# Kernel tuning notes

Measured on AMD Instinct MI355X. Metric: run time of the kernel, lower is better.

Reference implementation:

```python
import jax, jax.numpy as jnp
import numpy as np

B, N, FEAT, HID, K, GH, GW = 4, 4096, 64, 128, 16, 256, 256


def setup_inputs() -> dict:
    key = jax.random.key(0)
    ks = jax.random.split(key, 16)
    # N distinct grid cells per batch -> unique sparse coordinates (scn active sites)
    cells = jax.vmap(lambda k: jax.random.permutation(k, GH * GW)[:N])(jax.random.split(ks[0], B))
    cy = (cells // GW).astype(jnp.float32)
    cx = (cells % GW).astype(jnp.float32)
    x = cx / GW  # round(x*GW) == cx exactly
    y = cy / GH
    z = jnp.zeros((B, N), jnp.float32)
    p = jax.random.uniform(ks[1], (B, N), jnp.float32)
    xyzp = jnp.stack([x, y, z, p], axis=-1).astype(jnp.float32)
    features = jax.random.normal(ks[2], (B, N, FEAT), jnp.float32)

    def w(k, shape, s=0.05):
        return (jax.random.normal(k, shape) * s).astype(jnp.float32)

    return {
        "xyzp": xyzp, "features": features,
        "ln_g": jnp.ones((FEAT + 2,), jnp.float32), "ln_b": jnp.zeros((FEAT + 2,), jnp.float32),
        "W1": w(ks[3], (9, FEAT + 2, HID)), "b1": jnp.zeros((HID,), jnp.float32),
        "W2": w(ks[4], (9, HID, 3 * HID)),
        "pe_w1": w(ks[5], (3, HID)), "pe_b1": jnp.zeros((HID,), jnp.float32),
        "pe_w2": w(ks[6], (HID, HID)), "pe_b2": jnp.zeros((HID,), jnp.float32),
        "at_w1": w(ks[7], (HID, HID)), "at_b1": jnp.zeros((HID,), jnp.float32),
        "at_w2": w(ks[8], (HID, HID)), "at_b2": jnp.zeros((HID,), jnp.float32),
        "ag_w": w(ks[9], (HID, FEAT)), "ag_b": jnp.zeros((FEAT,), jnp.float32),
        "mlp_w1": w(ks[10], (FEAT, HID)), "mlp_b1": jnp.zeros((HID,), jnp.float32),
        "mlp_w2": w(ks[11], (HID, FEAT)), "mlp_b2": jnp.zeros((FEAT,), jnp.float32),
    }


def _knn_gather(xf, idx):
    # xf: [B,N,C], idx: [B,N,K] -> [B,N,K,C]
    return xf[jnp.arange(xf.shape[0])[:, None, None], idx]


def _forward(xyzp, features, ln_g, ln_b, W1, b1, W2, pe_w1, pe_b1, pe_w2, pe_b2,
             at_w1, at_b1, at_w2, at_b2, ag_w, ag_b, mlp_w1, mlp_b1, mlp_w2, mlp_b2):
    # knn in (x,y,0) space -> 2D squared distances, K nearest (self included, sorted)
    xy = xyzp[..., :2]
    s = jnp.sum(xy * xy, axis=-1)
    d2 = s[:, :, None] + s[:, None, :] - 2.0 * jnp.einsum('bnd,bmd->bnm', xy, xy)
    idx = jax.lax.top_k(-d2, K)[1]  # [B,N,K]

    # positional encoding of (x,y,p) relative offsets
    xyp = jnp.stack([xyzp[..., 0], xyzp[..., 1], xyzp[..., 3]], axis=-1)  # [B,N,3]
    rel = xyp[:, :, None, :] - _knn_gather(xyp, idx)  # [B,N,K,3]
    pe = jax.nn.relu(rel @ pe_w1 + pe_b1) @ pe_w2 + pe_b2  # [B,N,K,HID]

    # polarity split + LayerNorm
    p = (xyzp[..., 3:4] - 0.5) / 0.5
    sp = jnp.concatenate([jnp.clip(p, 0.0, 1.0), -jnp.clip(p, -1.0, 0.0), features], axis=-1)
    mu = jnp.mean(sp, axis=-1, keepdims=True)
    var = jnp.var(sp, axis=-1, keepdims=True)
    sp = (sp - mu) / jnp.sqrt(var + 1e-5) * ln_g + ln_b  # [B,N,FEAT+2]

    # submanifold 3x3 conv x2 via dense index grid (active sites only)
    cy = jnp.round(xyzp[..., 1] * GH).astype(jnp.int32)
    cx = jnp.round(xyzp[..., 0] * GW).astype(jnp.int32)
    bb = jnp.broadcast_to(jnp.arange(B)[:, None], (B, N))
    grid = jnp.full((B, GH + 2, GW + 2), -1, jnp.int32)
    grid = grid.at[bb, cy + 1, cx + 1].set(jnp.broadcast_to(jnp.arange(N, dtype=jnp.int32)[None], (B, N)))
    off = jnp.arange(-1, 2)
    dy = jnp.repeat(off, 3)  # [9]
    dx = jnp.tile(off, 3)    # [9]
    bi = jnp.arange(B)[:, None, None]
    nbr = grid[bi, cy[:, :, None] + 1 + dy, cx[:, :, None] + 1 + dx]  # [B,N,9]
    mask = nbr >= 0
    safe = jnp.where(mask, nbr, 0)
    m = mask[..., None].astype(sp.dtype)

    g1 = sp[bi, safe] * m                                   # [B,N,9,FEAT+2]
    h1 = jnp.einsum('bnkc,kcd->bnd', g1, W1) + b1           # [B,N,HID]
    g2 = h1[bi, safe] * m                                   # [B,N,9,HID]
    h2 = jnp.einsum('bnkc,kcd->bnd', g2, W2)                # [B,N,3*HID]

    qkv = h2.reshape(B, N, HID, 3)  # matches torch reshape([B,N,-1,3])
    q = qkv[..., 0]
    kk = _knn_gather(qkv[..., 1], idx)
    v = _knn_gather(qkv[..., 2], idx)

    # subtraction-based vector attention scored by MLP, softmax over neighbors
    a = q[:, :, None] - kk + pe
    a = jax.nn.relu(a @ at_w1 + at_b1) @ at_w2 + at_b2
    a = jax.nn.softmax(a / jnp.sqrt(jnp.float32(HID)), axis=-2)

    res = jnp.einsum('bmnf,bmnf->bmf', a, v + pe)
    res = res @ ag_w + ag_b + features
    res = jax.nn.gelu(res @ mlp_w1 + mlp_b1, approximate=False) @ mlp_w2 + mlp_b2 + features
    return res


def reference(xyzp, features, ln_g, ln_b, W1, b1, W2, pe_w1, pe_b1, pe_w2, pe_b2,
              at_w1, at_b1, at_w2, at_b2, ag_w, ag_b, mlp_w1, mlp_b1, mlp_w2, mlp_b2):
    return _forward(xyzp, features, ln_g, ln_b, W1, b1, W2, pe_w1, pe_b1, pe_w2, pe_b2,
                    at_w1, at_b1, at_w2, at_b2, ag_w, ag_b, mlp_w1, mlp_b1, mlp_w2, mlp_b2)
```

## Files before the change

kernel.cpp:

```cpp
#include <hip/hip_runtime.h>
#include <math.h>

#define BB 4
#define NN 4096
#define FEAT 64
#define HID 128
#define KNN 16
#define GS 258
#define CIN 66

typedef __attribute__((ext_vector_type(8))) short bf16x8;
typedef __attribute__((ext_vector_type(4))) float f32x4;
#define MFMA_B16(a, b, c) __builtin_amdgcn_mfma_f32_16x16x32_bf16(a, b, c, 0, 0, 0)

__device__ __forceinline__ short f2b(float f) {
    unsigned u = __builtin_bit_cast(unsigned, f);
    u = (u + 0x7FFFu + ((u >> 16) & 1u)) >> 16;
    return (short)u;
}
__device__ __forceinline__ float b2f(short s) {
    return __builtin_bit_cast(float, ((unsigned)(unsigned short)s) << 16);
}
__device__ __forceinline__ void gload_lds16(const void* g, void* lds) {
    __builtin_amdgcn_global_load_lds((const __attribute__((address_space(1))) unsigned int*)g,
                                     (__attribute__((address_space(3))) unsigned int*)lds, 16, 0, 0);
}

__global__ void k_scatter(const float* __restrict__ xyzp, int* __restrict__ grid, int* __restrict__ cxy) {
    int i = blockIdx.x * 256 + threadIdx.x;
    if (i >= BB * NN) return;
    int b = i / NN;
    float x = xyzp[(size_t)i * 4 + 0], y = xyzp[(size_t)i * 4 + 1];
    int cx = __float2int_rn(x * 256.0f);
    int cy = __float2int_rn(y * 256.0f);
    cxy[i] = cx | (cy << 8);
    grid[b * GS * GS + (cy + 1) * GS + (cx + 1)] = i % NN;
}

__device__ __forceinline__ void ins16(unsigned* a, unsigned key) {
    if (key < a[15]) {
#pragma unroll
        for (int j = 15; j >= 1; --j) {
            unsigned prev = a[j - 1];
            a[j] = (prev > key) ? prev : ((a[j] > key) ? key : a[j]);
        }
        a[0] = a[0] < key ? a[0] : key;
    }
}

__device__ __forceinline__ void cmpex(unsigned& x, unsigned& y) {
    unsigned lo = x < y ? x : y;
    unsigned hi = x < y ? y : x;
    x = lo; y = hi;
}

__device__ __forceinline__ void merge16(const unsigned* L, unsigned* c) {
#pragma unroll
    for (int i = 0; i < 16; ++i) c[i] = L[i];
#pragma unroll
    for (int s = 0; s < 4; ++s) {
        int m = 1 << s;
        unsigned bv[16];
#pragma unroll
        for (int i = 0; i < 16; ++i) bv[i] = __shfl_xor(c[15 - i], m);
#pragma unroll
        for (int i = 0; i < 16; ++i) c[i] = c[i] < bv[i] ? c[i] : bv[i];
#pragma unroll
        for (int d = 8; d >= 1; d >>= 1)
#pragma unroll
            for (int i = 0; i < 16; ++i)
                if (!(i & d)) cmpex(c[i], c[i | d]);
    }
}

__global__ __launch_bounds__(256) void k_knn(const int* __restrict__ grid, const int* __restrict__ cxy,
                                             const float* __restrict__ xyzp, float4* __restrict__ relg) {
    int tid = threadIdx.x;
    int t = tid & 15;
    int q = blockIdx.x * 16 + (tid >> 4);
    int b = q >> 12;
    int me = cxy[q];
    int mx = me & 255, my = (me >> 8) & 255;
    const int* gb = grid + b * GS * GS;
    unsigned L[16];
#pragma unroll
    for (int j = 0; j < 16; j++) L[j] = 0xFFFFFFFFu;
    for (int i = t; i < 441; i += 16) {
        int dy = i / 21 - 10, dx = i % 21 - 10;
        int Y = my + dy, X = mx + dx;
        if ((unsigned)Y >= 256u || (unsigned)X >= 256u) continue;
        int j = gb[(Y + 1) * GS + X + 1];
        if (j >= 0) ins16(L, ((unsigned)(dx * dx + dy * dy) << 12) | (unsigned)j);
    }
    unsigned c[16];
    merge16(L, c);
    for (int r = 11; r <= 256; ++r) {
        bool need = (c[15] >> 12) >= (unsigned)(r * r);
        if (!__any(need)) break;
        if (need) {
            int rr = r * r;
            for (int dx = -r + t; dx <= r; dx += 16) {
                int X = mx + dx;
                if ((unsigned)X >= 256u) continue;
                int d2t = dx * dx + rr;
                int Y0 = my - r, Y1 = my + r;
                if ((unsigned)Y0 < 256u) {
                    int j = gb[(Y0 + 1) * GS + X + 1];
                    if (j >= 0) ins16(L, ((unsigned)d2t << 12) | (unsigned)j);
                }
                if ((unsigned)Y1 < 256u) {
                    int j = gb[(Y1 + 1) * GS + X + 1];
                    if (j >= 0) ins16(L, ((unsigned)d2t << 12) | (unsigned)j);
                }
            }
            for (int dy = -r + 1 + t; dy <= r - 1; dy += 16) {
                int Y = my + dy;
                if ((unsigned)Y >= 256u) continue;
                int rowoff = (Y + 1) * GS;
                int d2s = rr + dy * dy;
                int X0 = mx - r, X1 = mx + r;
                if ((unsigned)X0 < 256u) {
                    int j = gb[rowoff + X0 + 1];
                    if (j >= 0) ins16(L, ((unsigned)d2s << 12) | (unsigned)j);
                }
                if ((unsigned)X1 < 256u) {
                    int j = gb[rowoff + X1 + 1];
                    if (j >= 0) ins16(L, ((unsigned)d2s << 12) | (unsigned)j);
                }
            }
            merge16(L, c);
        }
    }
    unsigned mine = 0;
#pragma unroll
    for (int j = 0; j < 16; ++j)
        if (t == j) mine = c[j];
    int g = (b << 12) | (int)(mine & 4095u);
    float4 mef = *(const float4*)(xyzp + (size_t)q * 4);
    float4 tt = *(const float4*)(xyzp + (size_t)g * 4);
    float4 o;
    o.x = mef.x - tt.x; o.y = mef.y - tt.y; o.z = mef.w - tt.w;
    o.w = __int_as_float(g);
    relg[(size_t)q * 16 + t] = o;
}

#define PK128_SZ (4 * 8 * 512)
#define PKW1_SZ (9 * 3 * 8 * 512)
#define PKW2_SZ (9 * 4 * 24 * 512)

__global__ __launch_bounds__(256) void k_pack(const float* __restrict__ pe_w2, const float* __restrict__ at_w1,
                                              const float* __restrict__ at_w2, const float* __restrict__ W1,
                                              const float* __restrict__ W2,
                                              short* __restrict__ pk_pe2, short* __restrict__ pk_a1,
                                              short* __restrict__ pk_a2, short* __restrict__ pk_w1,
                                              short* __restrict__ pk_w2) {
    int i = blockIdx.x * 256 + threadIdx.x;
    if (i < 3 * PK128_SZ) {
        int seg = i / PK128_SZ, r = i % PK128_SZ;
        int f = r / 512, q = r % 512;
        int lane = q / 8, j = q % 8;
        int kt = f / 8, nt = f % 8;
        int k = kt * 32 + (lane >> 4) * 8 + j, n = nt * 16 + (lane & 15);
        const float* W = (seg == 0) ? pe_w2 : (seg == 1) ? at_w1 : at_w2;
        short* dst = (seg == 0) ? pk_pe2 : (seg == 1) ? pk_a1 : pk_a2;
        dst[r] = f2b(W[k * 128 + n]);
        return;
    }
    i -= 3 * PK128_SZ;
    if (i < PKW1_SZ) {
        int f = i / 512, q = i % 512;
        int lane = q / 8, j = q % 8;
        int tap = f / 24, rem = f % 24;
        int kt = rem / 8, nt = rem % 8;
        int k = kt * 32 + (lane >> 4) * 8 + j, n = nt * 16 + (lane & 15);
        pk_w1[i] = (k < CIN) ? f2b(W1[(tap * CIN + k) * 128 + n]) : (short)0;
        return;
    }
    i -= PKW1_SZ;
    if (i < PKW2_SZ) {
        int f = i / 512, q = i % 512;
        int lane = q / 8, j = q % 8;
        int tap = f / 96, rem = f % 96;
        int kt = rem / 24, nt = rem % 24;
        int k = kt * 32 + (lane >> 4) * 8 + j, n = nt * 16 + (lane & 15);
        pk_w2[i] = f2b(W2[((size_t)(tap * 128 + k)) * 384 + n]);
    }
}

__global__ __launch_bounds__(256) void k_fold(const float* __restrict__ pe_w2, const float* __restrict__ at_w1,
                                              const float* __restrict__ pe_b2, const float* __restrict__ at_b1,
                                              short* __restrict__ pk_wf, float* __restrict__ cf) {
    int bid = blockIdx.x;
    if (bid == 64) {
        int j = threadIdx.x;
        if (j < 128) {
            float acc = at_b1[j];
            for (int m = 0; m < 128; ++m) acc += pe_b2[m] * at_w1[m * 128 + j];
            cf[j] = acc;
        }
        return;
    }
    int idx = bid * 256 + threadIdx.x;
    int i = idx >> 7, j = idx & 127;
    float acc = 0.f;
    for (int m = 0; m < 128; ++m) acc += pe_w2[i * 128 + m] * at_w1[m * 128 + j];
    int lane = (((i >> 3) & 3) << 4) | (j & 15);
    int dst = ((i >> 5) * 8 + (j >> 4)) * 512 + lane * 8 + (i & 7);
    pk_wf[dst] = f2b(acc);
}

__global__ __launch_bounds__(256) void k_sp(const float* __restrict__ xyzp, const float* __restrict__ feat,
                                            const float* __restrict__ ln_g, const float* __restrict__ ln_b,
                                            short* __restrict__ sp_bf) {
    int i = blockIdx.x * 256 + threadIdx.x;
    if (i >= BB * NN) return;
    float v[CIN];
    float p = xyzp[(size_t)i * 4 + 3];
    float pn = (p - 0.5f) * 2.0f;
    v[0] = fminf(fmaxf(pn, 0.0f), 1.0f);
    v[1] = -fminf(fmaxf(pn, -1.0f), 0.0f);
    const float4* f4 = (const float4*)(feat + (size_t)i * FEAT);
#pragma unroll
    for (int j = 0; j < FEAT / 4; j++) {
        float4 t = f4[j];
        v[2 + 4 * j] = t.x; v[3 + 4 * j] = t.y; v[4 + 4 * j] = t.z; v[5 + 4 * j] = t.w;
    }
    float s = 0.0f;
#pragma unroll
    for (int j = 0; j < CIN; j++) s += v[j];
    float mu = s / (float)CIN;
    float vs = 0.0f;
#pragma unroll
    for (int j = 0; j < CIN; j++) { float d = v[j] - mu; vs += d * d; }
    float inv = 1.0f / sqrtf(vs / (float)CIN + 1e-5f);
    unsigned o2[64];
#pragma unroll
    for (int j = 0; j < 33; j++) {
        float a = (v[2 * j] - mu) * inv * ln_g[2 * j] + ln_b[2 * j];
        float bqq = (2 * j + 1 < CIN) ? ((v[2 * j + 1] - mu) * inv * ln_g[2 * j + 1] + ln_b[2 * j + 1]) : 0.f;
        o2[j] = (unsigned)(unsigned short)f2b(a) | (((unsigned)(unsigned short)f2b(bqq)) << 16);
    }
#pragma unroll
    for (int j = 33; j < 64; j++) o2[j] = 0;
    int4* o = (int4*)(sp_bf + (size_t)i * 128);
#pragma unroll
    for (int t = 0; t < 16; t++) o[t] = make_int4(o2[4 * t], o2[4 * t + 1], o2[4 * t + 2], o2[4 * t + 3]);
}

__global__ __launch_bounds__(256) void k_conv1(const int* __restrict__ grid, const int* __restrict__ cxy,
                                               const short* __restrict__ sp_bf, const float* __restrict__ b1,
                                               const short* __restrict__ pk_w1, const short* __restrict__ zero256,
                                               short* __restrict__ h1_bf) {
    __shared__ int sj[9][64];
    __shared__ __align__(16) char sb[2][64 * 256];
    int row0 = blockIdx.x * 64;
    int b = row0 / NN;
    int tid = threadIdx.x;
    int w = tid >> 6, l = tid & 63, cl = l & 15;
    for (int e = tid; e < 9 * 64; e += 256) {
        int k = e / 64, p = e % 64;
        int me = cxy[row0 + p];
        sj[k][p] = grid[b * GS * GS + (((me >> 8) & 255) + k / 3) * GS + ((me & 255) + k % 3)];
    }
    __syncthreads();
    f32x4 acc[4][2];
#pragma unroll
    for (int m = 0; m < 4; m++)
#pragma unroll
        for (int nt = 0; nt < 2; nt++) acc[m][nt] = (f32x4){0.f, 0.f, 0.f, 0.f};

#define STAGE1(bufp, tap)                                                                      \
    {                                                                                          \
        _Pragma("unroll") for (int i = 0; i < 4; ++i) {                                        \
            int row = w * 16 + i * 4 + (l >> 4);                                               \
            int j = sj[tap][row];                                                              \
            int srcch = cl ^ (row & 7);                                                        \
            const short* src = (j >= 0) ? (sp_bf + ((size_t)(b * NN + j) * 128 + srcch * 8))   \
                                        : (zero256 + srcch * 8);                               \
            gload_lds16(src, (bufp) + (w * 16 + i * 4) * 256);                                 \
        }                                                                                      \
    }
    STAGE1(&sb[0][0], 0);
    asm volatile("s_waitcnt vmcnt(0)" ::: "memory");
    __syncthreads();
    int cur = 0;
    for (int tap = 0; tap < 9; ++tap) {
        if (tap < 8) STAGE1(&sb[cur ^ 1][0], tap + 1);
        const char* base = &sb[cur][0];
#pragma unroll
        for (int kt = 0; kt < 3; ++kt) {
            bf16x8 a[4];
#pragma unroll
            for (int m = 0; m < 4; ++m) {
                int row = m * 16 + (l & 15);
                a[m] = *(const bf16x8*)&base[row * 256 + ((kt * 64 + (l >> 4) * 16) ^ ((row & 7) << 4))];
            }
#pragma unroll
            for (int nt = 0; nt < 2; ++nt) {
                bf16x8 bv = *(const bf16x8*)(pk_w1 + (size_t)(((tap * 3 + kt) * 8 + w * 2 + nt) * 64 + l) * 8);
#pragma unroll
                for (int m = 0; m < 4; ++m) acc[m][nt] = MFMA_B16(a[m], bv, acc[m][nt]);
            }
        }
        asm volatile("s_waitcnt vmcnt(0)" ::: "memory");
        __syncthreads();
        cur ^= 1;
    }
#pragma unroll
    for (int nt = 0; nt < 2; ++nt) {
        int col = (w * 2 + nt) * 16 + cl;
        float bb = b1[col];
#pragma unroll
        for (int m = 0; m < 4; ++m)
#pragma unroll
            for (int j = 0; j < 4; ++j) {
                int row = row0 + m * 16 + (l >> 4) * 4 + j;
                h1_bf[(size_t)row * 128 + col] = f2b(acc[m][nt][j] + bb);
            }
    }
}

__global__ __launch_bounds__(256) void k_conv2(const int* __restrict__ grid, const int* __restrict__ cxy,
                                               const short* __restrict__ h1_bf, const short* __restrict__ pk_w2,
                                               const short* __restrict__ zero256,
                                               short* __restrict__ qg, short* __restrict__ kg, short* __restrict__ vg) {
    __shared__ int sj[9][64];
    __shared__ __align__(16) char sb[2][64 * 256];
    int bid = blockIdx.x;
    int nb = bid % 3, mb = bid / 3;
    int row0 = mb * 64;
    int b = row0 / NN;
    int tid = threadIdx.x;
    int w = tid >> 6, l = tid & 63, cl = l & 15;
    for (int e = tid; e < 9 * 64; e += 256) {
        int k = e / 64, p = e % 64;
        int me = cxy[row0 + p];
        sj[k][p] = grid[b * GS * GS + (((me >> 8) & 255) + k / 3) * GS + ((me & 255) + k % 3)];
    }
    __syncthreads();
    f32x4 acc[4][2];
#pragma unroll
    for (int m = 0; m < 4; m++)
#pragma unroll
        for (int nt = 0; nt < 2; nt++) acc[m][nt] = (f32x4){0.f, 0.f, 0.f, 0.f};

#define STAGE2(bufp, tap)                                                                      \
    {                                                                                          \
        _Pragma("unroll") for (int i = 0; i < 4; ++i) {                                        \
            int row = w * 16 + i * 4 + (l >> 4);                                               \
            int j = sj[tap][row];                                                              \
            int srcch = cl ^ (row & 7);                                                        \
            const short* src = (j >= 0) ? (h1_bf + ((size_t)(b * NN + j) * 128 + srcch * 8))   \
                                        : (zero256 + srcch * 8);                               \
            gload_lds16(src, (bufp) + (w * 16 + i * 4) * 256);                                 \
        }                                                                                      \
    }
    STAGE2(&sb[0][0], 0);
    asm volatile("s_waitcnt vmcnt(0)" ::: "memory");
    __syncthreads();
    int cur = 0;
    for (int tap = 0; tap < 9; ++tap) {
        if (tap < 8) STAGE2(&sb[cur ^ 1][0], tap + 1);
        const char* base = &sb[cur][0];
#pragma unroll
        for (int kt = 0; kt < 4; ++kt) {
            bf16x8 a[4];
#pragma unroll
            for (int m = 0; m < 4; ++m) {
                int row = m * 16 + (l & 15);
                a[m] = *(const bf16x8*)&base[row * 256 + ((kt * 64 + (l >> 4) * 16) ^ ((row & 7) << 4))];
            }
#pragma unroll
            for (int nt = 0; nt < 2; ++nt) {
                bf16x8 bv = *(const bf16x8*)(pk_w2 + (size_t)(((tap * 4 + kt) * 24 + nb * 8 + w * 2 + nt) * 64 + l) * 8);
#pragma unroll
                for (int m = 0; m < 4; ++m) acc[m][nt] = MFMA_B16(a[m], bv, acc[m][nt]);
            }
        }
        asm volatile("s_waitcnt vmcnt(0)" ::: "memory");
        __syncthreads();
        cur ^= 1;
    }
#pragma unroll
    for (int nt = 0; nt < 2; ++nt) {
        int col = nb * 128 + (w * 2 + nt) * 16 + cl;
        int s = col % 3, dd = col / 3;
#pragma unroll
        for (int m = 0; m < 4; ++m)
#pragma unroll
            for (int j = 0; j < 4; ++j) {
                int row = row0 + m * 16 + (l >> 4) * 4 + j;
                if (s == 0) qg[(size_t)row * 128 + dd] = f2b(acc[m][nt][j]);
                else if (s == 1) kg[(size_t)row * 128 + dd] = f2b(acc[m][nt][j]);
                else vg[(size_t)row * 128 + (dd & 15) * 8 + (dd >> 4)] = f2b(acc[m][nt][j]);
            }
    }
}

__global__ __launch_bounds__(256) void k_qk1(const short* __restrict__ qg, const short* __restrict__ kg,
                                             const short* __restrict__ pk_a1, const float* __restrict__ cf,
                                             short* __restrict__ q1, short* __restrict__ k1) {
    __shared__ __align__(16) char sb[64 * 256];
    int bid = blockIdx.x;
    int qmode = (bid < 256);
    int row0 = (bid & 255) * 64;
    const short* S = qmode ? qg : kg;
    short* O = qmode ? q1 : k1;
    int tid = threadIdx.x;
    int w = tid >> 6, l = tid & 63, cl = l & 15;
    for (int e = tid; e < 1024; e += 256) {
        int row = e >> 4, sl = e & 15;
        gload_lds16(S + ((size_t)(row0 + row) * 128 + (sl ^ (row & 7)) * 8), &sb[e * 16]);
    }
    asm volatile("s_waitcnt vmcnt(0)" ::: "memory");
    __syncthreads();
    f32x4 acc[4][2];
#pragma unroll
    for (int m = 0; m < 4; m++)
#pragma unroll
        for (int nt = 0; nt < 2; nt++) acc[m][nt] = (f32x4){0.f, 0.f, 0.f, 0.f};
#pragma unroll
    for (int kt = 0; kt < 4; ++kt) {
        bf16x8 a[4];
#pragma unroll
        for (int m = 0; m < 4; ++m) {
            int row = m * 16 + (l & 15);
            a[m] = *(const bf16x8*)&sb[row * 256 + ((kt * 64 + (l >> 4) * 16) ^ ((row & 7) << 4))];
        }
#pragma unroll
        for (int nt = 0; nt < 2; ++nt) {
            bf16x8 bv = *(const bf16x8*)(pk_a1 + (size_t)((kt * 8 + w * 2 + nt) * 64 + l) * 8);
#pragma unroll
            for (int m = 0; m < 4; ++m) acc[m][nt] = MFMA_B16(a[m], bv, acc[m][nt]);
        }
    }
#pragma unroll
    for (int nt = 0; nt < 2; ++nt) {
        int a = w * 2 + nt;
        int col = a * 16 + cl;
        float cv = qmode ? cf[col] : 0.f;
#pragma unroll
        for (int m = 0; m < 4; ++m)
#pragma unroll
            for (int j = 0; j < 4; ++j) {
                int row = row0 + m * 16 + (l >> 4) * 4 + j;
                O[(size_t)row * 128 + cl * 8 + a] = f2b(acc[m][nt][j] + cv);
            }
    }
}

__global__ __launch_bounds__(256, 3) void k_attn(const float4* __restrict__ relg,
                                                 const short* __restrict__ q1g, const short* __restrict__ k1g,
                                                 const short* __restrict__ vg,
                                                 const float* __restrict__ pe_w1, const float* __restrict__ pe_b1,
                                                 const float* __restrict__ pe_b2, const float* __restrict__ at_b2,
                                                 const short* __restrict__ pk_pe2, const short* __restrict__ pk_wf,
                                                 const short* __restrict__ pk_a2, float* __restrict__ res1) {
    __shared__ __align__(16) char s_work[4 * 4096];
    __shared__ float4 s_rel[64];
    int tid = threadIdx.x;
    int w = tid >> 6, l = tid & 63, cl = l & 15;
    int P = blockIdx.x * 4 + w;
    char* WK = s_work + w * 4096;

    int g_reg = 0;
    if (l < 16) {
        float4 f4 = relg[(size_t)P * 16 + l];
        s_rel[w * 16 + l] = f4;
        g_reg = __float_as_int(f4.w);
    }
    bf16x8 k1f[4], vf[4];
#pragma unroll
    for (int j = 0; j < 4; ++j) {
        int g = __shfl(g_reg, (l >> 4) * 4 + j);
        k1f[j] = *(const bf16x8*)(k1g + (size_t)g * 128 + cl * 8);
        vf[j] = *(const bf16x8*)(vg + (size_t)g * 128 + cl * 8);
    }
    bf16x8 q1f = *(const bf16x8*)(q1g + (size_t)P * 128 + cl * 8);
    {
        int c0 = 2 * l;
        float wa0 = pe_w1[c0], wa1 = pe_w1[c0 + 1];
        float wb0 = pe_w1[128 + c0], wb1 = pe_w1[129 + c0];
        float wc0 = pe_w1[256 + c0], wc1 = pe_w1[257 + c0];
        float ba0 = pe_b1[c0], ba1 = pe_b1[c0 + 1];
#pragma unroll
        for (int lr = 0; lr < 16; ++lr) {
            float4 rel = s_rel[w * 16 + lr];
            float h0 = fmaxf(rel.x * wa0 + rel.y * wb0 + rel.z * wc0 + ba0, 0.f);
            float h1v = fmaxf(rel.x * wa1 + rel.y * wb1 + rel.z * wc1 + ba1, 0.f);
            unsigned pk = (unsigned)(unsigned short)f2b(h0) | (((unsigned)(unsigned short)f2b(h1v)) << 16);
            *(unsigned*)&WK[lr * 256 + ((4 * l) ^ ((lr & 7) << 4))] = pk;
        }
    }
    int ra = l & 15;
    unsigned pe_pk[8][2];
    {
        f32x4 pacc[8];
#pragma unroll
        for (int nt = 0; nt < 8; nt++) pacc[nt] = (f32x4){0.f, 0.f, 0.f, 0.f};
#pragma unroll
        for (int kt = 0; kt < 4; ++kt) {
            int off = kt * 64 + (l >> 4) * 16;
            bf16x8 a0 = *(const bf16x8*)&WK[ra * 256 + (off ^ ((ra & 7) << 4))];
#pragma unroll
            for (int nt = 0; nt < 8; ++nt) {
                bf16x8 bv = *(const bf16x8*)(pk_pe2 + (size_t)((kt * 8 + nt) * 64 + l) * 8);
                pacc[nt] = MFMA_B16(a0, bv, pacc[nt]);
            }
        }
#pragma unroll
        for (int nt = 0; nt < 8; ++nt) {
            float b2v = pe_b2[nt * 16 + cl];
            float p0v = pacc[nt][0] + b2v, p1v = pacc[nt][1] + b2v;
            float p2v = pacc[nt][2] + b2v, p3v = pacc[nt][3] + b2v;
            pe_pk[nt][0] = (unsigned)(unsigned short)f2b(p0v) | (((unsigned)(unsigned short)f2b(p1v)) << 16);
            pe_pk[nt][1] = (unsigned)(unsigned short)f2b(p2v) | (((unsigned)(unsigned short)f2b(p3v)) << 16);
        }
    }
    f32x4 facc[8];
#pragma unroll
    for (int nt = 0; nt < 8; nt++) facc[nt] = (f32x4){0.f, 0.f, 0.f, 0.f};
#pragma unroll
    for (int kt = 0; kt < 4; ++kt) {
        int off = kt * 64 + (l >> 4) * 16;
        bf16x8 a0 = *(const bf16x8*)&WK[ra * 256 + (off ^ ((ra & 7) << 4))];
#pragma unroll
        for (int nt = 0; nt < 8; ++nt) {
            bf16x8 bv = *(const bf16x8*)(pk_wf + (size_t)((kt * 8 + nt) * 64 + l) * 8);
            facc[nt] = MFMA_B16(a0, bv, facc[nt]);
        }
    }
#pragma unroll
    for (int nt = 0; nt < 8; ++nt) {
        int col = nt * 16 + cl;
        float qv = b2f(q1f[nt]);
#pragma unroll
        for (int j = 0; j < 4; ++j) {
            int lr = (l >> 4) * 4 + j;
            float x = facc[nt][j] + qv - b2f(k1f[j][nt]);
            *(short*)&WK[lr * 256 + ((col * 2) ^ ((lr & 7) << 4))] = f2b(fmaxf(x, 0.f));
        }
    }
#pragma unroll
    for (int nt = 0; nt < 8; nt++) facc[nt] = (f32x4){0.f, 0.f, 0.f, 0.f};
#pragma unroll
    for (int kt = 0; kt < 4; ++kt) {
        int off = kt * 64 + (l >> 4) * 16;
        bf16x8 a0 = *(const bf16x8*)&WK[ra * 256 + (off ^ ((ra & 7) << 4))];
#pragma unroll
        for (int nt = 0; nt < 8; ++nt) {
            bf16x8 bv = *(const bf16x8*)(pk_a2 + (size_t)((kt * 8 + nt) * 64 + l) * 8);
            facc[nt] = MFMA_B16(a0, bv, facc[nt]);
        }
    }
    const float scale = 0.08838834764831845f;
#pragma unroll
    for (int nt = 0; nt < 8; ++nt) {
        int col = nt * 16 + cl;
        float bv = at_b2[col];
        float vv[4];
#pragma unroll
        for (int j = 0; j < 4; ++j) vv[j] = (facc[nt][j] + bv) * scale;
        float m = fmaxf(fmaxf(vv[0], vv[1]), fmaxf(vv[2], vv[3]));
        m = fmaxf(m, __shfl_xor(m, 16));
        m = fmaxf(m, __shfl_xor(m, 32));
        float ee[4], es = 0.f;
#pragma unroll
        for (int j = 0; j < 4; ++j) { ee[j] = __expf(vv[j] - m); es += ee[j]; }
        es += __shfl_xor(es, 16);
        es += __shfl_xor(es, 32);
        float pev[4];
        pev[0] = b2f((short)(pe_pk[nt][0] & 0xffff));
        pev[1] = b2f((short)(pe_pk[nt][0] >> 16));
        pev[2] = b2f((short)(pe_pk[nt][1] & 0xffff));
        pev[3] = b2f((short)(pe_pk[nt][1] >> 16));
        float o = 0.f;
#pragma unroll
        for (int j = 0; j < 4; ++j) o += ee[j] * (b2f(vf[j][nt]) + pev[j]);
        o += __shfl_xor(o, 16);
        o += __shfl_xor(o, 32);
        if (l < 16) res1[(size_t)P * 128 + col] = o / es;
    }
}

__global__ __launch_bounds__(256) void k_head(const float* __restrict__ res1, const float* __restrict__ feat,
                                              const float* __restrict__ ag_w, const float* __restrict__ ag_b,
                                              const float* __restrict__ mlp_w1, const float* __restrict__ mlp_b1,
                                              const float* __restrict__ mlp_w2, const float* __restrict__ mlp_b2,
                                              float* __restrict__ out) {
    __shared__ __align__(16) float rs[64][128];
    __shared__ __align__(16) float r1s[64][64];
    int tid = threadIdx.x;
    int i0 = blockIdx.x * 64;
    for (int e = tid; e < 64 * 128; e += 256) rs[e >> 7][e & 127] = res1[(size_t)i0 * 128 + e];
    __syncthreads();
    {
        int d = tid & 63, rg = tid >> 6;
        float acc[16];
#pragma unroll
        for (int i = 0; i < 16; i++) acc[i] = 0.0f;
        for (int c4 = 0; c4 < 32; ++c4) {
            int c = c4 * 4;
            float w0 = ag_w[c * 64 + d], w1 = ag_w[(c + 1) * 64 + d];
            float w2 = ag_w[(c + 2) * 64 + d], w3 = ag_w[(c + 3) * 64 + d];
#pragma unroll
            for (int i = 0; i < 16; i++) {
                float4 f = *(const float4*)&rs[rg * 16 + i][c];
                acc[i] += f.x * w0 + f.y * w1 + f.z * w2 + f.w * w3;
            }
        }
        float bb = ag_b[d];
#pragma unroll
        for (int i = 0; i < 16; i++) {
            int pp = rg * 16 + i;
            r1s[pp][d] = acc[i] + bb + feat[(size_t)(i0 + pp) * 64 + d];
        }
    }
    __syncthreads();
    {
        int d = tid & 127, rg = tid >> 7;
        float acc[32];
#pragma unroll
        for (int i = 0; i < 32; i++) acc[i] = 0.0f;
        for (int c4 = 0; c4 < 16; ++c4) {
            int c = c4 * 4;
            float w0 = mlp_w1[c * 128 + d], w1 = mlp_w1[(c + 1) * 128 + d];
            float w2 = mlp_w1[(c + 2) * 128 + d], w3 = mlp_w1[(c + 3) * 128 + d];
#pragma unroll
            for (int i = 0; i < 32; i++) {
                float4 f = *(const float4*)&r1s[rg * 32 + i][c];
                acc[i] += f.x * w0 + f.y * w1 + f.z * w2 + f.w * w3;
            }
        }
        float bb = mlp_b1[d];
#pragma unroll
        for (int i = 0; i < 32; i++) {
            float x = acc[i] + bb;
            rs[rg * 32 + i][d] = 0.5f * x * (1.0f + erff(x * 0.70710678118654752f));
        }
    }
    __syncthreads();
    {
        int d = tid & 63, rg = tid >> 6;
        float acc[16];
#pragma unroll
        for (int i = 0; i < 16; i++) acc[i] = 0.0f;
        for (int c4 = 0; c4 < 32; ++c4) {
            int c = c4 * 4;
            float w0 = mlp_w2[c * 64 + d], w1 = mlp_w2[(c + 1) * 64 + d];
            float w2 = mlp_w2[(c + 2) * 64 + d], w3 = mlp_w2[(c + 3) * 64 + d];
#pragma unroll
            for (int i = 0; i < 16; i++) {
                float4 f = *(const float4*)&rs[rg * 16 + i][c];
                acc[i] += f.x * w0 + f.y * w1 + f.z * w2 + f.w * w3;
            }
        }
        float bb = mlp_b2[d];
#pragma unroll
        for (int i = 0; i < 16; i++) {
            int pp = rg * 16 + i;
            out[(size_t)(i0 + pp) * 64 + d] = acc[i] + bb + feat[(size_t)(i0 + pp) * 64 + d];
        }
    }
}

extern "C" void kernel_launch(void* const* d_in, const int* in_sizes, int n_in,
                              void* d_out, int out_size, void* d_ws, size_t ws_size,
                              hipStream_t stream) {
    const float* xyzp = (const float*)d_in[0];
    const float* features = (const float*)d_in[1];
    const float* ln_g = (const float*)d_in[2];
    const float* ln_b = (const float*)d_in[3];
    const float* W1 = (const float*)d_in[4];
    const float* b1 = (const float*)d_in[5];
    const float* W2 = (const float*)d_in[6];
    const float* pe_w1 = (const float*)d_in[7];
    const float* pe_b1 = (const float*)d_in[8];
    const float* pe_w2 = (const float*)d_in[9];
    const float* pe_b2 = (const float*)d_in[10];
    const float* at_w1 = (const float*)d_in[11];
    const float* at_b1 = (const float*)d_in[12];
    const float* at_w2 = (const float*)d_in[13];
    const float* at_b2 = (const float*)d_in[14];
    const float* ag_w = (const float*)d_in[15];
    const float* ag_b = (const float*)d_in[16];
    const float* mlp_w1 = (const float*)d_in[17];
    const float* mlp_b1 = (const float*)d_in[18];
    const float* mlp_w2 = (const float*)d_in[19];
    const float* mlp_b2 = (const float*)d_in[20];
    float* out = (float*)d_out;

    char* w = (char*)d_ws;
    auto alloc = [&](size_t bytes) { char* pp = w; w += (bytes + 255) & ~(size_t)255; return pp; };
    int* grid = (int*)alloc((size_t)BB * GS * GS * 4);
    short* zero256 = (short*)alloc(256);
    int* cxy = (int*)alloc((size_t)BB * NN * 4);
    float4* relg = (float4*)alloc((size_t)BB * NN * KNN * 16);
    short* sp_bf = (short*)alloc((size_t)BB * NN * 128 * 2);
    short* h1_bf = (short*)alloc((size_t)BB * NN * HID * 2);
    short* qg = (short*)alloc((size_t)BB * NN * HID * 2);
    short* kg = (short*)alloc((size_t)BB * NN * HID * 2);
    short* vg = (short*)alloc((size_t)BB * NN * HID * 2);
    short* q1 = (short*)alloc((size_t)BB * NN * HID * 2);
    short* k1 = (short*)alloc((size_t)BB * NN * HID * 2);
    float* res1 = (float*)alloc((size_t)BB * NN * HID * 4);
    short* pk_pe2 = (short*)alloc((size_t)PK128_SZ * 2);
    short* pk_a1 = (short*)alloc((size_t)PK128_SZ * 2);
    short* pk_a2 = (short*)alloc((size_t)PK128_SZ * 2);
    short* pk_wf = (short*)alloc((size_t)PK128_SZ * 2);
    short* pk_w1 = (short*)alloc((size_t)PKW1_SZ * 2);
    short* pk_w2 = (short*)alloc((size_t)PKW2_SZ * 2);
    float* cf = (float*)alloc(128 * 4);

    hipMemsetAsync(grid, 0xFF, (size_t)BB * GS * GS * 4, stream);
    hipMemsetAsync(zero256, 0, 256, stream);
    k_scatter<<<(BB * NN + 255) / 256, 256, 0, stream>>>(xyzp, grid, cxy);
    k_pack<<<(3 * PK128_SZ + PKW1_SZ + PKW2_SZ + 255) / 256, 256, 0, stream>>>(
        pe_w2, at_w1, at_w2, W1, W2, pk_pe2, pk_a1, pk_a2, pk_w1, pk_w2);
    k_fold<<<65, 256, 0, stream>>>(pe_w2, at_w1, pe_b2, at_b1, pk_wf, cf);
    k_knn<<<BB * NN / 16, 256, 0, stream>>>(grid, cxy, xyzp, relg);
    k_sp<<<(BB * NN + 255) / 256, 256, 0, stream>>>(xyzp, features, ln_g, ln_b, sp_bf);
    k_conv1<<<BB * NN / 64, 256, 0, stream>>>(grid, cxy, sp_bf, b1, pk_w1, zero256, h1_bf);
    k_conv2<<<(BB * NN / 64) * 3, 256, 0, stream>>>(grid, cxy, h1_bf, pk_w2, zero256, qg, kg, vg);
    k_qk1<<<512, 256, 0, stream>>>(qg, kg, pk_a1, cf, q1, k1);
    k_attn<<<BB * NN / 4, 256, 0, stream>>>(relg, q1, k1, vg, pe_w1, pe_b1, pe_b2, at_b2,
                                            pk_pe2, pk_wf, pk_a2, res1);
    k_head<<<BB * NN / 64, 256, 0, stream>>>(res1, features, ag_w, ag_b, mlp_w1, mlp_b1, mlp_w2, mlp_b2, out);
}
```

Baseline: 241.5 us.

## Share attention MLP tiles across block waves and drop transposed k/v layouts

The attention kernel no longer has each wave handle one point's 16 neighbours across all 128 columns. All four waves now share a 64-row LDS tile, and each wave computes a 32-column slice for all four points, so every B-fragment load of the weights feeds four MFMAs instead of one. The k1, q1 and v buffers switch to plain row-major layout, and the kernel gathers scalar bf16 values per lane instead of 16-byte vectors. This cuts global weight-fragment traffic but adds block-wide barriers and many narrow 2-byte gathers.

```diff
diff --git a/kernel.cpp b/kernel.cpp
--- a/kernel.cpp
+++ b/kernel.cpp
@@ -385,14 +385,13 @@
     for (int nt = 0; nt < 2; ++nt) {
         int col = nb * 128 + (w * 2 + nt) * 16 + cl;
         int s = col % 3, dd = col / 3;
+        short* dst = (s == 0) ? qg : (s == 1) ? kg : vg;
 #pragma unroll
         for (int m = 0; m < 4; ++m)
 #pragma unroll
             for (int j = 0; j < 4; ++j) {
                 int row = row0 + m * 16 + (l >> 4) * 4 + j;
-                if (s == 0) qg[(size_t)row * 128 + dd] = f2b(acc[m][nt][j]);
-                else if (s == 1) kg[(size_t)row * 128 + dd] = f2b(acc[m][nt][j]);
-                else vg[(size_t)row * 128 + (dd & 15) * 8 + (dd >> 4)] = f2b(acc[m][nt][j]);
+                dst[(size_t)row * 128 + dd] = f2b(acc[m][nt][j]);
             }
     }
 }
@@ -436,15 +435,14 @@
     }
 #pragma unroll
     for (int nt = 0; nt < 2; ++nt) {
-        int a = w * 2 + nt;
-        int col = a * 16 + cl;
+        int col = (w * 2 + nt) * 16 + cl;
         float cv = qmode ? cf[col] : 0.f;
 #pragma unroll
         for (int m = 0; m < 4; ++m)
 #pragma unroll
             for (int j = 0; j < 4; ++j) {
                 int row = row0 + m * 16 + (l >> 4) * 4 + j;
-                O[(size_t)row * 128 + cl * 8 + a] = f2b(acc[m][nt][j] + cv);
+                O[(size_t)row * 128 + col] = f2b(acc[m][nt][j] + cv);
             }
     }
 }
@@ -456,27 +454,18 @@
                                                  const float* __restrict__ pe_b2, const float* __restrict__ at_b2,
                                                  const short* __restrict__ pk_pe2, const short* __restrict__ pk_wf,
                                                  const short* __restrict__ pk_a2, float* __restrict__ res1) {
-    __shared__ __align__(16) char s_work[4 * 4096];
+    __shared__ __align__(16) char WK[64 * 256];
     __shared__ float4 s_rel[64];
+    __shared__ int s_g[64];
     int tid = threadIdx.x;
     int w = tid >> 6, l = tid & 63, cl = l & 15;
-    int P = blockIdx.x * 4 + w;
-    char* WK = s_work + w * 4096;
-
-    int g_reg = 0;
+    int P0 = blockIdx.x * 4;
+
     if (l < 16) {
-        float4 f4 = relg[(size_t)P * 16 + l];
+        float4 f4 = relg[(size_t)(P0 + w) * 16 + l];
         s_rel[w * 16 + l] = f4;
-        g_reg = __float_as_int(f4.w);
-    }
-    bf16x8 k1f[4], vf[4];
-#pragma unroll
-    for (int j = 0; j < 4; ++j) {
-        int g = __shfl(g_reg, (l >> 4) * 4 + j);
-        k1f[j] = *(const bf16x8*)(k1g + (size_t)g * 128 + cl * 8);
-        vf[j] = *(const bf16x8*)(vg + (size_t)g * 128 + cl * 8);
-    }
-    bf16x8 q1f = *(const bf16x8*)(q1g + (size_t)P * 128 + cl * 8);
+        s_g[w * 16 + l] = __float_as_int(f4.w);
+    }
     {
         int c0 = 2 * l;
         float wa0 = pe_w1[c0], wa1 = pe_w1[c0 + 1];
@@ -489,98 +478,156 @@
             float h0 = fmaxf(rel.x * wa0 + rel.y * wb0 + rel.z * wc0 + ba0, 0.f);
             float h1v = fmaxf(rel.x * wa1 + rel.y * wb1 + rel.z * wc1 + ba1, 0.f);
             unsigned pk = (unsigned)(unsigned short)f2b(h0) | (((unsigned)(unsigned short)f2b(h1v)) << 16);
-            *(unsigned*)&WK[lr * 256 + ((4 * l) ^ ((lr & 7) << 4))] = pk;
-        }
-    }
-    int ra = l & 15;
-    unsigned pe_pk[8][2];
+            *(unsigned*)&WK[(w * 16 + lr) * 256 + ((4 * l) ^ ((lr & 7) << 4))] = pk;
+        }
+    }
+    __syncthreads();
+    unsigned short k1v[4][2][4];
+    unsigned short q1v[4][2];
+#pragma unroll
+    for (int m = 0; m < 4; ++m) {
+#pragma unroll
+        for (int j = 0; j < 4; ++j) {
+            int g = s_g[m * 16 + (l >> 4) * 4 + j];
+#pragma unroll
+            for (int nt = 0; nt < 2; ++nt)
+                k1v[m][nt][j] = *((const unsigned short*)k1g + (size_t)g * 128 + w * 32 + nt * 16 + cl);
+        }
+#pragma unroll
+        for (int nt = 0; nt < 2; ++nt)
+            q1v[m][nt] = *((const unsigned short*)q1g + (size_t)(P0 + m) * 128 + w * 32 + nt * 16 + cl);
+    }
+    unsigned pe_pk[4][2][2];
     {
-        f32x4 pacc[8];
-#pragma unroll
-        for (int nt = 0; nt < 8; nt++) pacc[nt] = (f32x4){0.f, 0.f, 0.f, 0.f};
+        f32x4 pacc[4][2];
+#pragma unroll
+        for (int m = 0; m < 4; m++)
+#pragma unroll
+            for (int nt = 0; nt < 2; nt++) pacc[m][nt] = (f32x4){0.f, 0.f, 0.f, 0.f};
 #pragma unroll
         for (int kt = 0; kt < 4; ++kt) {
             int off = kt * 64 + (l >> 4) * 16;
-            bf16x8 a0 = *(const bf16x8*)&WK[ra * 256 + (off ^ ((ra & 7) << 4))];
-#pragma unroll
-            for (int nt = 0; nt < 8; ++nt) {
-                bf16x8 bv = *(const bf16x8*)(pk_pe2 + (size_t)((kt * 8 + nt) * 64 + l) * 8);
-                pacc[nt] = MFMA_B16(a0, bv, pacc[nt]);
-            }
-        }
-#pragma unroll
-        for (int nt = 0; nt < 8; ++nt) {
-            float b2v = pe_b2[nt * 16 + cl];
-            float p0v = pacc[nt][0] + b2v, p1v = pacc[nt][1] + b2v;
-            float p2v = pacc[nt][2] + b2v, p3v = pacc[nt][3] + b2v;
-            pe_pk[nt][0] = (unsigned)(unsigned short)f2b(p0v) | (((unsigned)(unsigned short)f2b(p1v)) << 16);
-            pe_pk[nt][1] = (unsigned)(unsigned short)f2b(p2v) | (((unsigned)(unsigned short)f2b(p3v)) << 16);
-        }
-    }
-    f32x4 facc[8];
-#pragma unroll
-    for (int nt = 0; nt < 8; nt++) facc[nt] = (f32x4){0.f, 0.f, 0.f, 0.f};
+            bf16x8 a[4];
+#pragma unroll
+            for (int m = 0; m < 4; ++m) {
+                int ra = m * 16 + (l & 15);
+                a[m] = *(const bf16x8*)&WK[ra * 256 + (off ^ ((ra & 7) << 4))];
+            }
+#pragma unroll
+            for (int nt = 0; nt < 2; ++nt) {
+                bf16x8 bv = *(const bf16x8*)(pk_pe2 + (size_t)((kt * 8 + w * 2 + nt) * 64 + l) * 8);
+#pragma unroll
+                for (int m = 0; m < 4; ++m) pacc[m][nt] = MFMA_B16(a[m], bv, pacc[m][nt]);
+            }
+        }
+#pragma unroll
+        for (int nt = 0; nt < 2; ++nt) {
+            float b2v = pe_b2[w * 32 + nt * 16 + cl];
+#pragma unroll
+            for (int m = 0; m < 4; ++m) {
+                float p0v = pacc[m][nt][0] + b2v, p1v = pacc[m][nt][1] + b2v;
+                float p2v = pacc[m][nt][2] + b2v, p3v = pacc[m][nt][3] + b2v;
+                pe_pk[m][nt][0] = (unsigned)(unsigned short)f2b(p0v) | (((unsigned)(unsigned short)f2b(p1v)) << 16);
+                pe_pk[m][nt][1] = (unsigned)(unsigned short)f2b(p2v) | (((unsigned)(unsigned short)f2b(p3v)) << 16);
+            }
+        }
+    }
+    f32x4 facc[4][2];
+#pragma unroll
+    for (int m = 0; m < 4; m++)
+#pragma unroll
+        for (int nt = 0; nt < 2; nt++) facc[m][nt] = (f32x4){0.f, 0.f, 0.f, 0.f};
 #pragma unroll
     for (int kt = 0; kt < 4; ++kt) {
         int off = kt * 64 + (l >> 4) * 16;
-        bf16x8 a0 = *(const bf16x8*)&WK[ra * 256 + (off ^ ((ra & 7) << 4))];
-#pragma unroll
-        for (int nt = 0; nt < 8; ++nt) {
-            bf16x8 bv = *(const bf16x8*)(pk_wf + (size_t)((kt * 8 + nt) * 64 + l) * 8);
-            facc[nt] = MFMA_B16(a0, bv, facc[nt]);
-        }
-    }
-#pragma unroll
-    for (int nt = 0; nt < 8; ++nt) {
-        int col = nt * 16 + cl;
-        float qv = b2f(q1f[nt]);
+        bf16x8 a[4];
+#pragma unroll
+        for (int m = 0; m < 4; ++m) {
+            int ra = m * 16 + (l & 15);
+            a[m] = *(const bf16x8*)&WK[ra * 256 + (off ^ ((ra & 7) << 4))];
+        }
+#pragma unroll
+        for (int nt = 0; nt < 2; ++nt) {
+            bf16x8 bv = *(const bf16x8*)(pk_wf + (size_t)((kt * 8 + w * 2 + nt) * 64 + l) * 8);
+#pragma unroll
+            for (int m = 0; m < 4; ++m) facc[m][nt] = MFMA_B16(a[m], bv, facc[m][nt]);
+        }
+    }
+    __syncthreads();
+#pragma unroll
+    for (int m = 0; m < 4; ++m)
+#pragma unroll
+        for (int nt = 0; nt < 2; ++nt) {
+            int col = w * 32 + nt * 16 + cl;
+            float qv = b2f((short)q1v[m][nt]);
+#pragma unroll
+            for (int j = 0; j < 4; ++j) {
+                int rr = m * 16 + (l >> 4) * 4 + j;
+                float x = facc[m][nt][j] + qv - b2f((short)k1v[m][nt][j]);
+                *(short*)&WK[rr * 256 + ((col * 2) ^ ((rr & 7) << 4))] = f2b(fmaxf(x, 0.f));
+            }
+        }
+    unsigned short vv[4][2][4];
+#pragma unroll
+    for (int m = 0; m < 4; ++m)
 #pragma unroll
         for (int j = 0; j < 4; ++j) {
-            int lr = (l >> 4) * 4 + j;
-            float x = facc[nt][j] + qv - b2f(k1f[j][nt]);
-            *(short*)&WK[lr * 256 + ((col * 2) ^ ((lr & 7) << 4))] = f2b(fmaxf(x, 0.f));
-        }
-    }
-#pragma unroll
-    for (int nt = 0; nt < 8; nt++) facc[nt] = (f32x4){0.f, 0.f, 0.f, 0.f};
+            int g = s_g[m * 16 + (l >> 4) * 4 + j];
+#pragma unroll
+            for (int nt = 0; nt < 2; ++nt)
+                vv[m][nt][j] = *((const unsigned short*)vg + (size_t)g * 128 + w * 32 + nt * 16 + cl);
+        }
+    __syncthreads();
+#pragma unroll
+    for (int m = 0; m < 4; m++)
+#pragma unroll
+        for (int nt = 0; nt < 2; nt++) facc[m][nt] = (f32x4){0.f, 0.f, 0.f, 0.f};
 #pragma unroll
     for (int kt = 0; kt < 4; ++kt) {
         int off = kt * 64 + (l >> 4) * 16;
-        bf16x8 a0 = *(const bf16x8*)&WK[ra * 256 + (off ^ ((ra & 7) << 4))];
-#pragma unroll
-        for (int nt = 0; nt < 8; ++nt) {
-            bf16x8 bv = *(const bf16x8*)(pk_a2 + (size_t)((kt * 8 + nt) * 64 + l) * 8);
-            facc[nt] = MFMA_B16(a0, bv, facc[nt]);
+        bf16x8 a[4];
+#pragma unroll
+        for (int m = 0; m < 4; ++m) {
+            int ra = m * 16 + (l & 15);
+            a[m] = *(const bf16x8*)&WK[ra * 256 + (off ^ ((ra & 7) << 4))];
+        }
+#pragma unroll
+        for (int nt = 0; nt < 2; ++nt) {
+            bf16x8 bv = *(const bf16x8*)(pk_a2 + (size_t)((kt * 8 + w * 2 + nt) * 64 + l) * 8);
+#pragma unroll
+            for (int m = 0; m < 4; ++m) facc[m][nt] = MFMA_B16(a[m], bv, facc[m][nt]);
         }
     }
     const float scale = 0.08838834764831845f;
 #pragma unroll
-    for (int nt = 0; nt < 8; ++nt) {
-        int col = nt * 16 + cl;
-        float bv = at_b2[col];
-        float vv[4];
-#pragma unroll
-        for (int j = 0; j < 4; ++j) vv[j] = (facc[nt][j] + bv) * scale;
-        float m = fmaxf(fmaxf(vv[0], vv[1]), fmaxf(vv[2], vv[3]));
-        m = fmaxf(m, __shfl_xor(m, 16));
-        m = fmaxf(m, __shfl_xor(m, 32));
-        float ee[4], es = 0.f;
-#pragma unroll
-        for (int j = 0; j < 4; ++j) { ee[j] = __expf(vv[j] - m); es += ee[j]; }
-        es += __shfl_xor(es, 16);
-        es += __shfl_xor(es, 32);
-        float pev[4];
-        pev[0] = b2f((short)(pe_pk[nt][0] & 0xffff));
-        pev[1] = b2f((short)(pe_pk[nt][0] >> 16));
-        pev[2] = b2f((short)(pe_pk[nt][1] & 0xffff));
-        pev[3] = b2f((short)(pe_pk[nt][1] >> 16));
-        float o = 0.f;
-#pragma unroll
-        for (int j = 0; j < 4; ++j) o += ee[j] * (b2f(vf[j][nt]) + pev[j]);
-        o += __shfl_xor(o, 16);
-        o += __shfl_xor(o, 32);
-        if (l < 16) res1[(size_t)P * 128 + col] = o / es;
-    }
+    for (int m = 0; m < 4; ++m)
+#pragma unroll
+        for (int nt = 0; nt < 2; ++nt) {
+            int col = w * 32 + nt * 16 + cl;
+            float bv = at_b2[col];
+            float sv[4];
+#pragma unroll
+            for (int j = 0; j < 4; ++j) sv[j] = (facc[m][nt][j] + bv) * scale;
+            float mx = fmaxf(fmaxf(sv[0], sv[1]), fmaxf(sv[2], sv[3]));
+            mx = fmaxf(mx, __shfl_xor(mx, 16));
+            mx = fmaxf(mx, __shfl_xor(mx, 32));
+            float ee[4], es = 0.f;
+#pragma unroll
+            for (int j = 0; j < 4; ++j) { ee[j] = __expf(sv[j] - mx); es += ee[j]; }
+            es += __shfl_xor(es, 16);
+            es += __shfl_xor(es, 32);
+            float pev[4];
+            pev[0] = b2f((short)(pe_pk[m][nt][0] & 0xffff));
+            pev[1] = b2f((short)(pe_pk[m][nt][0] >> 16));
+            pev[2] = b2f((short)(pe_pk[m][nt][1] & 0xffff));
+            pev[3] = b2f((short)(pe_pk[m][nt][1] >> 16));
+            float o = 0.f;
+#pragma unroll
+            for (int j = 0; j < 4; ++j) o += ee[j] * (b2f((short)vv[m][nt][j]) + pev[j]);
+            o += __shfl_xor(o, 16);
+            o += __shfl_xor(o, 32);
+            if (l < 16) res1[(size_t)(P0 + m) * 128 + col] = o / es;
+        }
 }
 
 __global__ __launch_bounds__(256) void k_head(const float* __restrict__ res1, const float* __restrict__ feat,
```

Measured after the change: 213.9 us. 11.4% less time.
